# Kernel tuning notes

Hardware: AMD Instinct MI355X
Metric: run time of the kernel (lower is better)

The kernel has to match this reference:

```python
import jax, jax.numpy as jnp
import numpy as np

TOP_K = 2

def setup_inputs() -> dict:
    key = jax.random.key(0)
    k1, k2, k3 = jax.random.split(key, 3)
    B, D, E = 32768, 768, 8
    h = jax.random.normal(k1, (B, D), dtype=jnp.float32)
    gate_w = jax.random.normal(k2, (E, D), dtype=jnp.float32) * 0.02
    gate_b = jax.random.normal(k3, (E,), dtype=jnp.float32) * 0.02
    return {"h": h, "gate_w": gate_w, "gate_b": gate_b}

def reference(h, gate_w, gate_b):
    # logits: [B, n_experts] = h @ W^T + b
    logits = jnp.einsum('bd,ed->be', h, gate_w) + gate_b
    # top-k over experts (eval path: no jitter noise)
    top_vals, indices = jax.lax.top_k(logits, TOP_K)   # [B, top_k]
    weights = jax.nn.softmax(top_vals, axis=-1)        # [B, top_k]
    return indices, weights, logits
```

## Files before the change

kernel.cpp:

```cpp
#include <hip/hip_runtime.h>
#include <hip/hip_bf16.h>
#include <math.h>


constexpr int D  = 768;
constexpr int E  = 8;
constexpr int D4 = D / 4;
constexpr int BLOCK  = 256;
constexpr int GRID_A = 512;

__device__ __forceinline__ float dot4acc(float4 a, float4 b, float acc) {
    acc = fmaf(a.x, b.x, acc);
    acc = fmaf(a.y, b.y, acc);
    acc = fmaf(a.z, b.z, acc);
    acc = fmaf(a.w, b.w, acc);
    return acc;
}

__device__ __forceinline__ float wave_reduce8(float a[8], int lane) {
    {
        const bool hi = lane & 1;
#pragma unroll
        for (int j = 0; j < 4; ++j) {
            float send = hi ? a[j] : a[j + 4];
            float recv = __shfl_xor(send, 1, 64);
            float keep = hi ? a[j + 4] : a[j];
            a[j] = keep + recv;
        }
    }
    {
        const bool hi = lane & 2;
#pragma unroll
        for (int j = 0; j < 2; ++j) {
            float send = hi ? a[j] : a[j + 2];
            float recv = __shfl_xor(send, 2, 64);
            float keep = hi ? a[j + 2] : a[j];
            a[j] = keep + recv;
        }
    }
    {
        const bool hi = lane & 4;
        float send = hi ? a[0] : a[1];
        float recv = __shfl_xor(send, 4, 64);
        float keep = hi ? a[1] : a[0];
        a[0] = keep + recv;
    }
    float v = a[0];
    v += __shfl_xor(v, 8, 64);
    v += __shfl_xor(v, 16, 64);
    v += __shfl_xor(v, 32, 64);
    return v;
}

__device__ __forceinline__ void load_pair(float4 dst[6], const float4* __restrict__ h4,
                                          int pair, int lane) {
    const float4* hp = h4 + (size_t)pair * (2 * D4) + lane;
#pragma unroll
    for (int c = 0; c < 3; ++c) dst[c]     = hp[c * 64];
#pragma unroll
    for (int c = 0; c < 3; ++c) dst[3 + c] = hp[D4 + c * 64];
}

__global__ __launch_bounds__(BLOCK, 2)
void router_logits_kernel(const float* __restrict__ h,
                          const float* __restrict__ gate_w,
                          const float* __restrict__ gate_b,
                          float* __restrict__ out_logits,
                          int B) {
    const int tid    = threadIdx.x;
    const int lane   = tid & 63;
    const int wave   = tid >> 6;
    const int gwave  = blockIdx.x * (BLOCK / 64) + wave;
    const int nwaves = gridDim.x * (BLOCK / 64);

    const int l3 = lane & 7;
    const int e_lane = ((l3 & 1) << 2) | (l3 & 2) | ((l3 >> 2) & 1);
    const float bias = gate_b[e_lane];

    const float4* gw4 = (const float4*)gate_w;
    float4 greg[24];
#pragma unroll
    for (int e = 0; e < E; ++e)
#pragma unroll
        for (int c = 0; c < 3; ++c)
            greg[e * 3 + c] = gw4[e * D4 + c * 64 + lane];

    const float4* h4 = (const float4*)h;
    const int npairs = B >> 1;

    int p = gwave;
    if (p >= npairs) return;

    float4 cv[6];
    load_pair(cv, h4, p, lane);

    while (true) {
        const int pn = p + nwaves;
        const bool more = (pn < npairs);

        float4 nv[6];
        if (more) load_pair(nv, h4, pn, lane);

        float acc0[E], acc1[E];
#pragma unroll
        for (int e = 0; e < E; ++e) { acc0[e] = 0.0f; acc1[e] = 0.0f; }

#pragma unroll
        for (int c = 0; c < 3; ++c) {
#pragma unroll
            for (int e = 0; e < E; ++e) {
                float4 g = greg[e * 3 + c];
                acc0[e] = dot4acc(cv[c],     g, acc0[e]);
                acc1[e] = dot4acc(cv[3 + c], g, acc1[e]);
            }
        }

        float va = wave_reduce8(acc0, lane) + bias;
        float vb = wave_reduce8(acc1, lane) + bias;

        float v = (lane & 8) ? vb : va;
        if (lane < 16) out_logits[(size_t)p * 16 + (lane & 8) + e_lane] = v;

        if (!more) break;
#pragma unroll
        for (int i = 0; i < 6; ++i) cv[i] = nv[i];
        p = pn;
    }
}

__global__ __launch_bounds__(BLOCK)
void router_topk_kernel(const float* __restrict__ logits,
                        float* __restrict__ out_idx,
                        float* __restrict__ out_w,
                        int B) {
    const int t = blockIdx.x * BLOCK + threadIdx.x;
    if (t >= B) return;

    const float4* lp = (const float4*)(logits + (size_t)t * 8);
    float4 a = lp[0], b = lp[1];
    float l[8] = {a.x, a.y, a.z, a.w, b.x, b.y, b.z, b.w};

    float v0 = l[0]; int i0 = 0;
    float v1 = -INFINITY; int i1 = -1;
#pragma unroll
    for (int e = 1; e < 8; ++e) {
        float x = l[e];
        bool gt0 = x > v0;
        bool gt1 = x > v1;
        float nv1 = gt0 ? v0 : (gt1 ? x : v1);
        int   ni1 = gt0 ? i0 : (gt1 ? e : i1);
        v1 = nv1; i1 = ni1;
        v0 = gt0 ? x : v0;
        i0 = gt0 ? e : i0;
    }
    float tt = expf(v1 - v0);
    float w0 = 1.0f / (1.0f + tt);
    float w1 = tt * w0;

    ((float2*)out_idx)[t] = make_float2((float)i0, (float)i1);
    ((float2*)out_w)[t]   = make_float2(w0, w1);
}

extern "C" void kernel_launch(void* const* d_in, const int* in_sizes, int n_in,
                              void* d_out, int out_size, void* d_ws, size_t ws_size,
                              hipStream_t stream) {
    const float* h      = (const float*)d_in[0];
    const float* gate_w = (const float*)d_in[1];
    const float* gate_b = (const float*)d_in[2];

    const int B = in_sizes[0] / D;

    float* out        = (float*)d_out;
    float* out_idx    = out;
    float* out_w      = out + (size_t)B * 2;
    float* out_logits = out + (size_t)B * 4;

    router_logits_kernel<<<dim3(GRID_A), dim3(BLOCK), 0, stream>>>(
        h, gate_w, gate_b, out_logits, B);

    router_topk_kernel<<<dim3((B + BLOCK - 1) / BLOCK), dim3(BLOCK), 0, stream>>>(
        out_logits, out_idx, out_w, B);
}
```

Baseline: 148.1 us.

## Stream hidden-state rows into LDS via async global_load_lds double buffering

Replaces the register-based prefetch of the next row pair with `__builtin_amdgcn_global_load_lds` DMA into a per-wave, double-buffered LDS staging area. The current buffer is read from LDS while the next pair is fetched directly into the other buffer. The aim is to keep more memory traffic in flight without tying up VGPRs. The logits grid also grows from 512 to 768 blocks, and the per-expert dot products are reordered into independent chains. In exchange it uses about 48KB of LDS per block and relies on the compiler inserting the right vmcnt waits before the LDS reads.

Result: no change. 148.4 us (+0.3%).

```diff
diff --git a/kernel.cpp b/kernel.cpp
--- a/kernel.cpp
+++ b/kernel.cpp
@@ -7,7 +7,11 @@
 constexpr int E  = 8;
 constexpr int D4 = D / 4;
 constexpr int BLOCK  = 256;
-constexpr int GRID_A = 512;
+constexpr int GRID_A = 768;
+constexpr int BLOCK_B = 256;
+
+typedef __attribute__((address_space(1))) const float4 gas_float4;
+typedef __attribute__((address_space(3))) float4 las_float4;
 
 __device__ __forceinline__ float dot4acc(float4 a, float4 b, float acc) {
     acc = fmaf(a.x, b.x, acc);
@@ -16,6 +20,9 @@
     acc = fmaf(a.w, b.w, acc);
     return acc;
 }
+__device__ __forceinline__ float dot4(float4 a, float4 b) {
+    return fmaf(a.x, b.x, fmaf(a.y, b.y, fmaf(a.z, b.z, a.w * b.w)));
+}
 
 __device__ __forceinline__ float wave_reduce8(float a[8], int lane) {
     {
@@ -52,13 +59,19 @@
     return v;
 }
 
-__device__ __forceinline__ void load_pair(float4 dst[6], const float4* __restrict__ h4,
-                                          int pair, int lane) {
-    const float4* hp = h4 + (size_t)pair * (2 * D4) + lane;
-#pragma unroll
-    for (int c = 0; c < 3; ++c) dst[c]     = hp[c * 64];
-#pragma unroll
-    for (int c = 0; c < 3; ++c) dst[3 + c] = hp[D4 + c * 64];
+__device__ __forceinline__ void dma_pair(const float4* __restrict__ h4, int p,
+                                         int lane, float4* lds_base) {
+    const float4* hp = h4 + (size_t)p * (2 * D4) + lane;
+#pragma unroll
+    for (int c = 0; c < 3; ++c)
+        __builtin_amdgcn_global_load_lds((gas_float4*)(hp + c * 64),
+                                         (las_float4*)(lds_base + c * 64),
+                                         16, 0, 0);
+#pragma unroll
+    for (int c = 0; c < 3; ++c)
+        __builtin_amdgcn_global_load_lds((gas_float4*)(hp + D4 + c * 64),
+                                         (las_float4*)(lds_base + 192 + c * 64),
+                                         16, 0, 0);
 }
 
 __global__ __launch_bounds__(BLOCK, 2)
@@ -67,6 +80,8 @@
                           const float* __restrict__ gate_b,
                           float* __restrict__ out_logits,
                           int B) {
+    __shared__ float4 hbuf[2][BLOCK / 64][2 * D4];
+
     const int tid    = threadIdx.x;
     const int lane   = tid & 63;
     const int wave   = tid >> 6;
@@ -91,28 +106,33 @@
     int p = gwave;
     if (p >= npairs) return;
 
-    float4 cv[6];
-    load_pair(cv, h4, p, lane);
+    int buf = 0;
+    dma_pair(h4, p, lane, &hbuf[0][wave][0]);
 
     while (true) {
         const int pn = p + nwaves;
         const bool more = (pn < npairs);
 
-        float4 nv[6];
-        if (more) load_pair(nv, h4, pn, lane);
+        float4 cv[6];
+        float4* cur = &hbuf[buf][wave][0];
+#pragma unroll
+        for (int c = 0; c < 3; ++c) cv[c]     = cur[c * 64 + lane];
+#pragma unroll
+        for (int c = 0; c < 3; ++c) cv[3 + c] = cur[192 + c * 64 + lane];
+
+        if (more) dma_pair(h4, pn, lane, &hbuf[buf ^ 1][wave][0]);
 
         float acc0[E], acc1[E];
 #pragma unroll
-        for (int e = 0; e < E; ++e) { acc0[e] = 0.0f; acc1[e] = 0.0f; }
-
-#pragma unroll
-        for (int c = 0; c < 3; ++c) {
-#pragma unroll
-            for (int e = 0; e < E; ++e) {
-                float4 g = greg[e * 3 + c];
-                acc0[e] = dot4acc(cv[c],     g, acc0[e]);
-                acc1[e] = dot4acc(cv[3 + c], g, acc1[e]);
-            }
+        for (int e = 0; e < E; ++e) {
+            float a0 = dot4(cv[0], greg[e * 3 + 0]);
+            a0 = dot4acc(cv[1], greg[e * 3 + 1], a0);
+            a0 = dot4acc(cv[2], greg[e * 3 + 2], a0);
+            acc0[e] = a0;
+            float a1 = dot4(cv[3], greg[e * 3 + 0]);
+            a1 = dot4acc(cv[4], greg[e * 3 + 1], a1);
+            a1 = dot4acc(cv[5], greg[e * 3 + 2], a1);
+            acc1[e] = a1;
         }
 
         float va = wave_reduce8(acc0, lane) + bias;
@@ -122,18 +142,17 @@
         if (lane < 16) out_logits[(size_t)p * 16 + (lane & 8) + e_lane] = v;
 
         if (!more) break;
-#pragma unroll
-        for (int i = 0; i < 6; ++i) cv[i] = nv[i];
         p = pn;
-    }
-}
-
-__global__ __launch_bounds__(BLOCK)
+        buf ^= 1;
+    }
+}
+
+__global__ __launch_bounds__(BLOCK_B)
 void router_topk_kernel(const float* __restrict__ logits,
                         float* __restrict__ out_idx,
                         float* __restrict__ out_w,
                         int B) {
-    const int t = blockIdx.x * BLOCK + threadIdx.x;
+    const int t = blockIdx.x * BLOCK_B + threadIdx.x;
     if (t >= B) return;
 
     const float4* lp = (const float4*)(logits + (size_t)t * 8);
@@ -178,6 +197,6 @@
     router_logits_kernel<<<dim3(GRID_A), dim3(BLOCK), 0, stream>>>(
         h, gate_w, gate_b, out_logits, B);
 
-    router_topk_kernel<<<dim3((B + BLOCK - 1) / BLOCK), dim3(BLOCK), 0, stream>>>(
+    router_topk_kernel<<<dim3((B + BLOCK_B - 1) / BLOCK_B), dim3(BLOCK_B), 0, stream>>>(
         out_logits, out_idx, out_w, B);
 }
```
